# Optimization experiments

Hardware: AMD Instinct MI355X
Metric: run time of the kernel (lower is better)

## Reference

```python
import jax, jax.numpy as jnp
import numpy as np

EPS = 1e-5


def _bn(x, w, b, m, v):
    # eval-mode BatchNorm2d over channel axis (NCHW)
    inv = w / jnp.sqrt(v + EPS)
    return x * inv[None, :, None, None] + (b - m * inv)[None, :, None, None]


def _conv(x, w, pad):
    return jax.lax.conv_general_dilated(
        x, w, window_strides=(1, 1), padding=[(pad, pad), (pad, pad)],
        dimension_numbers=('NCHW', 'OIHW', 'NCHW'))


def setup_inputs() -> dict:
    key = jax.random.key(0)
    ks = jax.random.split(key, 40)
    B, Cin, Cm, Cout, H, W = 4, 64, 64, 64, 64, 64
    C8 = Cm // 8
    d = {}
    d['x'] = jax.random.normal(ks[0], (B, Cin, H, W), jnp.float32)
    d['conv1_w'] = jax.random.normal(ks[1], (Cm, Cin, 3, 3), jnp.float32) * 0.05
    d['conv2_w'] = jax.random.normal(ks[2], (Cout, Cm, 3, 3), jnp.float32) * 0.05

    def bn_params(i, c):
        return (jax.random.normal(ks[i], (c,), jnp.float32) * 0.1 + 1.0,
                jax.random.normal(ks[i + 1], (c,), jnp.float32) * 0.1,
                jax.random.normal(ks[i + 2], (c,), jnp.float32) * 0.1,
                jax.random.uniform(ks[i + 3], (c,), jnp.float32) + 0.5)

    d['f_w'] = jax.random.normal(ks[3], (C8, Cm, 1, 1), jnp.float32) * 0.1
    d['f_b'] = jax.random.normal(ks[4], (C8,), jnp.float32) * 0.05
    d['f_bn_w'], d['f_bn_b'], d['f_bn_m'], d['f_bn_v'] = bn_params(5, C8)
    d['g_w'] = jax.random.normal(ks[9], (C8, Cm, 1, 1), jnp.float32) * 0.1
    d['g_b'] = jax.random.normal(ks[10], (C8,), jnp.float32) * 0.05
    d['g_bn_w'], d['g_bn_b'], d['g_bn_m'], d['g_bn_v'] = bn_params(11, C8)
    d['gamma'] = jax.random.normal(ks[15], (1,), jnp.float32) * 0.5
    d['h_w'] = jax.random.normal(ks[16], (C8, Cm, 1, 1), jnp.float32) * 0.1
    d['h_b'] = jax.random.normal(ks[17], (C8,), jnp.float32) * 0.05
    d['h_bn_w'], d['h_bn_b'], d['h_bn_m'], d['h_bn_v'] = bn_params(18, C8)
    d['i_w'] = jax.random.normal(ks[22], (Cm, C8, 1, 1), jnp.float32) * 0.1
    d['i_b'] = jax.random.normal(ks[23], (Cm,), jnp.float32) * 0.05
    d['i_bn_w'], d['i_bn_b'], d['i_bn_m'], d['i_bn_v'] = bn_params(24, Cm)
    return d


def reference(x, conv1_w, conv2_w,
              f_w, f_b, f_bn_w, f_bn_b, f_bn_m, f_bn_v,
              g_w, g_b, g_bn_w, g_bn_b, g_bn_m, g_bn_v,
              gamma, h_w, h_b, h_bn_w, h_bn_b, h_bn_m, h_bn_v,
              i_w, i_b, i_bn_w, i_bn_b, i_bn_m, i_bn_v):
    out = _conv(x, conv1_w, 1)                      # [B, Cm, W, H]
    B, Cm, Wd, Hd = out.shape
    C8 = Cm // 8
    N = Wd * Hd

    # SelfAttention: f/g 1x1-conv + BN projections -> [B,N,N] map, softmax over dim=1
    f = _bn(_conv(out, f_w, 0) + f_b[None, :, None, None], f_bn_w, f_bn_b, f_bn_m, f_bn_v)
    g = _bn(_conv(out, g_w, 0) + g_b[None, :, None, None], g_bn_w, g_bn_b, g_bn_m, g_bn_v)
    f = f.reshape(B, C8, N).transpose(0, 2, 1)      # [B, N, C8]
    g = g.reshape(B, C8, N)                         # [B, C8, N]
    att = jnp.einsum('bnc,bcm->bnm', f, g)          # [B, N, N]
    att = jax.nn.softmax(att, axis=1)               # torch softmax(att, 1)

    # SelfAttentionPost: gamma-scaled value projection, bmm, expand, BN, residual
    h = gamma * _bn(_conv(out, h_w, 0) + h_b[None, :, None, None], h_bn_w, h_bn_b, h_bn_m, h_bn_v)
    h = h.reshape(B, C8, N).transpose(0, 2, 1)      # [B, N, C8]
    h = jnp.einsum('bnm,bmc->bnc', att, h)          # [B, N, C8]
    h = h.reshape(B, Wd, Hd, C8).transpose(0, 3, 1, 2)  # [B, C8, W, H]
    out = _bn(_conv(h, i_w, 0) + i_b[None, :, None, None], i_bn_w, i_bn_b, i_bn_m, i_bn_v) + out

    return _conv(out, conv2_w, 1)
```

## Files before the change

### kernel.cpp

```cpp
#include <hip/hip_runtime.h>

#define EPSBN 1e-5f
#define L2E 1.44269504088896340736f

typedef __attribute__((ext_vector_type(4)))  float f32x4;
typedef __attribute__((ext_vector_type(16))) float f32x16;
typedef __attribute__((ext_vector_type(8)))  short bf16x8;

__device__ __forceinline__ unsigned short f2bf(float f) {
    unsigned u = __float_as_uint(f);
    u = (u + 0x7FFFu + ((u >> 16) & 1u)) >> 16;
    return (unsigned short)u;
}
__device__ __forceinline__ float bf2f(unsigned short h) {
    return __uint_as_float((unsigned)h << 16);
}
__device__ __forceinline__ unsigned cvt_pk_bf16(float lo, float hi) {
    unsigned r;
    asm("v_cvt_pk_bf16_f32 %0, %1, %2" : "=v"(r) : "v"(lo), "v"(hi));
    return r;
}

__global__ __launch_bounds__(256) void prep_k(
    const float* __restrict__ x, const float* __restrict__ w1,
    const float* __restrict__ w2,
    unsigned short* __restrict__ xT, unsigned short* __restrict__ wt1,
    unsigned short* __restrict__ wt2)
{
    const int tid = threadIdx.x;
    if (blockIdx.x < 256) {
        __shared__ unsigned short tls[64][72];
        const int b = blockIdx.x >> 6, p0 = (blockIdx.x & 63) << 6;
        const int ci = tid >> 2, pq = tid & 3;
        const float* src = x + (((size_t)(b * 64 + ci)) << 12) + p0 + pq * 16;
#pragma unroll
        for (int j = 0; j < 4; ++j) {
            const float4 v = *(const float4*)(src + j * 4);
            const int pl = pq * 16 + j * 4;
            tls[pl][ci]     = f2bf(v.x);
            tls[pl + 1][ci] = f2bf(v.y);
            tls[pl + 2][ci] = f2bf(v.z);
            tls[pl + 3][ci] = f2bf(v.w);
        }
        __syncthreads();
        const int pix = tid >> 2, cg = tid & 3;
        const uint4 a  = *(const uint4*)&tls[pix][cg << 4];
        const uint4 b2 = *(const uint4*)&tls[pix][(cg << 4) + 8];
        unsigned short* dst = xT + (((size_t)((b << 12) + p0 + pix)) << 6) + (cg << 4);
        *(uint4*)dst       = a;
        *(uint4*)(dst + 8) = b2;
    } else {
        const int e0 = (blockIdx.x - 256) * 2048 + tid * 8;
#pragma unroll
        for (int j = 0; j < 8; ++j) {
            const int e = e0 + j;
            const int which = e >= 36864;
            const int je = which ? e - 36864 : e;
            const int t_ = je >> 12, co = (je >> 6) & 63, ci = je & 63;
            const float val = (which ? w2 : w1)[(co * 64 + ci) * 9 + t_];
            (which ? wt2 : wt1)[je] = f2bf(val);
        }
    }
}

__global__ __launch_bounds__(256) void conv3x3_k(
    const unsigned short* __restrict__ xT, const unsigned short* __restrict__ wt,
    float* __restrict__ y)
{
    __shared__ unsigned short xs[3][66][72];
    __shared__ unsigned short ws[9][32][72];
    __shared__ float          ls[32][68];

    const int b  = blockIdx.z;
    const int cg = blockIdx.y;
    const int r0 = blockIdx.x;
    const int tid = threadIdx.x;

    for (int u = tid; u < 1536; u += 256) {
        const int kh = u >> 9, rem = u & 511;
        const int p = 1 + (rem >> 3), cig = rem & 7;
        const int gr = r0 + kh - 1;
        uint4 v = make_uint4(0u, 0u, 0u, 0u);
        if ((unsigned)gr < 64u)
            v = *(const uint4*)(xT + (((size_t)((b << 12) + (gr << 6) + (p - 1))) << 6) + (cig << 3));
        const int s = (p >> 3) & 7;
        *(uint4*)&xs[kh][p][(cig ^ s) << 3] = v;
    }
    if (tid < 48) {
        const int kh = tid >> 4, pp = (tid & 8) ? 65 : 0, cig = tid & 7;
        *(uint4*)&xs[kh][pp][cig << 3] = make_uint4(0u, 0u, 0u, 0u);
    }
    for (int u = tid; u < 2304; u += 256) {
        const int t_ = u >> 8, rem = u & 255;
        const int co = rem >> 3, cig = rem & 7;
        const uint4 v = *(const uint4*)(wt + (((t_ * 64) + (cg << 5) + co) << 6) + (cig << 3));
        *(uint4*)&ws[t_][co][cig << 3] = v;
    }
    __syncthreads();

    const int lane = tid & 63, grp = tid >> 6;
    const int lr = lane & 15, lk = lane >> 4;
    const int pixbase = (grp << 4) + lr;

    f32x4 acc0 = {0.f, 0.f, 0.f, 0.f};
    f32x4 acc1 = {0.f, 0.f, 0.f, 0.f};

#pragma unroll
    for (int t = 0; t < 9; ++t) {
        const int kh = t / 3, kw = t % 3;
        const int p  = pixbase + kw;
        const int sw = ((p >> 3) & 7) << 3;
#pragma unroll
        for (int ch = 0; ch < 2; ++ch) {
            const int cio = (ch << 5) + (lk << 3);
            const bf16x8 a  = *(const bf16x8*)&xs[kh][p][cio ^ sw];
            const bf16x8 b0 = *(const bf16x8*)&ws[t][lr][cio];
            const bf16x8 b1 = *(const bf16x8*)&ws[t][16 + lr][cio];
            acc0 = __builtin_amdgcn_mfma_f32_16x16x32_bf16(a, b0, acc0, 0, 0, 0);
            acc1 = __builtin_amdgcn_mfma_f32_16x16x32_bf16(a, b1, acc1, 0, 0, 0);
        }
    }

#pragma unroll
    for (int j = 0; j < 4; ++j) {
        const int pix = (grp << 4) + (lk << 2) + j;
        ls[lr][pix]      = acc0[j];
        ls[lr + 16][pix] = acc1[j];
    }
    __syncthreads();

    const int co_l = tid >> 3, pq = (tid & 7) << 3;
    float* yp = y + (((size_t)((b << 6) + (cg << 5) + co_l)) << 12) + (r0 << 6) + pq;
    *(float4*)yp       = *(const float4*)&ls[co_l][pq];
    *(float4*)(yp + 4) = *(const float4*)&ls[co_l][pq + 4];
}

__global__ __launch_bounds__(256) void proj_k(
    const float* __restrict__ out1,
    const float* __restrict__ f_w, const float* __restrict__ f_b,
    const float* __restrict__ f_bw, const float* __restrict__ f_bb,
    const float* __restrict__ f_bm, const float* __restrict__ f_bv,
    const float* __restrict__ g_w, const float* __restrict__ g_b,
    const float* __restrict__ g_bw, const float* __restrict__ g_bb,
    const float* __restrict__ g_bm, const float* __restrict__ g_bv,
    const float* __restrict__ h_w, const float* __restrict__ h_b,
    const float* __restrict__ h_bw, const float* __restrict__ h_bb,
    const float* __restrict__ h_bm, const float* __restrict__ h_bv,
    const float* __restrict__ gamma,
    unsigned short* __restrict__ fb, unsigned short* __restrict__ gb,
    float* __restrict__ hb)
{
    __shared__ float comb[3][64][25];

    const int pl = threadIdx.x >> 2, q = threadIdx.x & 3;
    const int pix = blockIdx.x * 64 + pl;
    const int b = pix >> 12, p = pix & 4095;
    const int cibase = q << 4;

    const float* xp = out1 + ((size_t)b << 18) + ((size_t)cibase << 12) + p;

    float aF[8], aG[8], aH[8];
#pragma unroll
    for (int c = 0; c < 8; ++c) { aF[c] = 0.f; aG[c] = 0.f; aH[c] = 0.f; }

#pragma unroll
    for (int ci = 0; ci < 16; ++ci) {
        const float xv = xp[(size_t)ci << 12];
#pragma unroll
        for (int c = 0; c < 8; ++c) {
            aF[c] = fmaf(xv, f_w[c * 64 + cibase + ci], aF[c]);
            aG[c] = fmaf(xv, g_w[c * 64 + cibase + ci], aG[c]);
            aH[c] = fmaf(xv, h_w[c * 64 + cibase + ci], aH[c]);
        }
    }

    if (q) {
        float* cp = comb[q - 1][pl];
#pragma unroll
        for (int c = 0; c < 8; ++c) { cp[c] = aF[c]; cp[8 + c] = aG[c]; cp[16 + c] = aH[c]; }
    }
    __syncthreads();
    if (q == 0) {
#pragma unroll
        for (int k = 0; k < 3; ++k) {
            const float* cp = comb[k][pl];
#pragma unroll
            for (int c = 0; c < 8; ++c) { aF[c] += cp[c]; aG[c] += cp[8 + c]; aH[c] += cp[16 + c]; }
        }

        const float gm = gamma[0];
        float fo[8], go[8], ho[8];
#pragma unroll
        for (int c = 0; c < 8; ++c) {
            float invf = f_bw[c] * rsqrtf(f_bv[c] + EPSBN);
            fo[c] = ((aF[c] + f_b[c]) * invf + (f_bb[c] - f_bm[c] * invf)) * L2E;
            float invg = g_bw[c] * rsqrtf(g_bv[c] + EPSBN);
            go[c] = (aG[c] + g_b[c]) * invg + (g_bb[c] - g_bm[c] * invg);
            float invh = h_bw[c] * rsqrtf(h_bv[c] + EPSBN);
            ho[c] = gm * ((aH[c] + h_b[c]) * invh + (h_bb[c] - h_bm[c] * invh));
        }

        unsigned short fhi[8], flo[8], ghi[8], glo[8];
#pragma unroll
        for (int c = 0; c < 8; ++c) {
            fhi[c] = f2bf(fo[c]);
            flo[c] = f2bf(fo[c] - bf2f(fhi[c]));
            ghi[c] = f2bf(go[c]);
            glo[c] = f2bf(go[c] - bf2f(ghi[c]));
        }
        uint4 fA, fB, gA, gB;
        fA.x = (unsigned)fhi[0] | ((unsigned)fhi[1] << 16);
        fA.y = (unsigned)fhi[2] | ((unsigned)fhi[3] << 16);
        fA.z = (unsigned)fhi[4] | ((unsigned)fhi[5] << 16);
        fA.w = (unsigned)fhi[6] | ((unsigned)fhi[7] << 16);
        fB.x = (unsigned)flo[0] | ((unsigned)flo[1] << 16);
        fB.y = (unsigned)flo[2] | ((unsigned)flo[3] << 16);
        fB.z = (unsigned)flo[4] | ((unsigned)flo[5] << 16);
        fB.w = (unsigned)flo[6] | ((unsigned)flo[7] << 16);
        gA.x = (unsigned)ghi[0] | ((unsigned)ghi[1] << 16);
        gA.y = (unsigned)ghi[2] | ((unsigned)ghi[3] << 16);
        gA.z = (unsigned)ghi[4] | ((unsigned)ghi[5] << 16);
        gA.w = (unsigned)ghi[6] | ((unsigned)ghi[7] << 16);
        gB.x = (unsigned)glo[0] | ((unsigned)glo[1] << 16);
        gB.y = (unsigned)glo[2] | ((unsigned)glo[3] << 16);
        gB.z = (unsigned)glo[4] | ((unsigned)glo[5] << 16);
        gB.w = (unsigned)glo[6] | ((unsigned)glo[7] << 16);

        *(uint4*)(fb + ((size_t)pix << 4))     = fA;
        *(uint4*)(fb + ((size_t)pix << 4) + 8) = fB;
        *(uint4*)(gb + ((size_t)pix << 4))     = gA;
        *(uint4*)(gb + ((size_t)pix << 4) + 8) = gB;

        float4* hp = (float4*)(hb + ((size_t)pix << 3));
        hp[0] = make_float4(ho[0], ho[1], ho[2], ho[3]);
        hp[1] = make_float4(ho[4], ho[5], ho[6], ho[7]);
    }
}

__global__ __launch_bounds__(256) void pass1_k(
    const unsigned short* __restrict__ fb, const unsigned short* __restrict__ gb,
    const float* __restrict__ hb, unsigned short* __restrict__ hT)
{
    __shared__ float Dp[4][2][16];
    __shared__ float Dscale[32];

    const int b = blockIdx.y;
    const int mtile0 = blockIdx.x << 5;
    const int tid = threadIdx.x;
    const int wv = tid >> 6, l = tid & 63, col = l & 31, hl = l >> 5;

    const bf16x8 Gf = *(const bf16x8*)(gb + (((size_t)(b * 4096 + mtile0 + col)) << 4) + (hl << 3));

    const f32x16 Z = {0.f, 0.f, 0.f, 0.f, 0.f, 0.f, 0.f, 0.f,
                      0.f, 0.f, 0.f, 0.f, 0.f, 0.f, 0.f, 0.f};
    float Dacc[16];
#pragma unroll
    for (int r = 0; r < 16; ++r) Dacc[r] = 0.f;

    const unsigned short* fbase = fb + (((size_t)(b * 4096 + (wv << 10))) << 4);

    for (int nc = 0; nc < 32; ++nc) {
        const unsigned short* fr = fbase + ((size_t)((nc << 5) + col) << 4);
        const bf16x8 Fhi = *(const bf16x8*)fr;
        const bf16x8 Flo = *(const bf16x8*)(fr + 8);
        f32x16 T = __builtin_amdgcn_mfma_f32_32x32x16_bf16(Gf, Fhi, Z, 0, 0, 0);
        T = __builtin_amdgcn_mfma_f32_32x32x16_bf16(Gf, Flo, T, 0, 0, 0);
#pragma unroll
        for (int r = 0; r < 16; ++r)
            Dacc[r] += __builtin_amdgcn_exp2f(T[r]);
    }

#pragma unroll
    for (int s = 1; s < 32; s <<= 1) {
#pragma unroll
        for (int r = 0; r < 16; ++r)
            Dacc[r] += __shfl_xor(Dacc[r], s);
    }

    if (col == 0) {
#pragma unroll
        for (int r = 0; r < 16; ++r) Dp[wv][hl][r] = Dacc[r];
    }
    __syncthreads();
    if (tid < 32) {
        const int r = tid & 15, h = tid >> 4;
        const float D = Dp[0][h][r] + Dp[1][h][r] + Dp[2][h][r] + Dp[3][h][r];
        const int m = (r & 3) + ((r >> 2) << 3) + (h << 2);
        Dscale[m] = 1.f / D;
    }
    __syncthreads();
    if (tid < 64) {
        const int ml = tid & 31, c0 = (tid >> 5) << 2;
        const float sc = Dscale[ml];
        const float4 hv = *(const float4*)(hb + (((size_t)(b * 4096 + mtile0 + ml)) << 3) + c0);
        unsigned short* o = hT + ((size_t)b << 15) + mtile0 + ml;
        o[(size_t)(c0    ) << 12] = f2bf(hv.x * sc);
        o[(size_t)(c0 + 1) << 12] = f2bf(hv.y * sc);
        o[(size_t)(c0 + 2) << 12] = f2bf(hv.z * sc);
        o[(size_t)(c0 + 3) << 12] = f2bf(hv.w * sc);
    }
}

__global__ __launch_bounds__(256) void pass2_k(
    const unsigned short* __restrict__ fb, const unsigned short* __restrict__ gb,
    const unsigned short* __restrict__ hT, float* __restrict__ o)
{
    __shared__ float red[4][64][4];

    const int b = blockIdx.y, nt = blockIdx.x;
    const int tid = threadIdx.x, wv = tid >> 6, l = tid & 63;
    const int col = l & 31;
    const bool lo = l < 32;
    const int hl8 = lo ? 0 : 8;

    const unsigned short* frow = fb + (((size_t)(b * 4096 + (nt << 5) + col)) << 4);
    const bf16x8 Fhi = *(const bf16x8*)frow;
    const bf16x8 Flo = *(const bf16x8*)(frow + 8);

    const f32x16 Z = {0.f, 0.f, 0.f, 0.f, 0.f, 0.f, 0.f, 0.f,
                      0.f, 0.f, 0.f, 0.f, 0.f, 0.f, 0.f, 0.f};
    f32x16 Oacc = Z;

    const unsigned short* hbase = hT + ((size_t)b << 15) + ((size_t)col << 12) + hl8;
    const bool hvalid = col < 8;

    for (int mci = 0; mci < 32; ++mci) {
        const int mc = (wv << 5) + mci;
        const bf16x8 Gf = *(const bf16x8*)(gb + (((size_t)(b * 4096 + (mc << 5) + col)) << 4) + hl8);
        f32x16 T = __builtin_amdgcn_mfma_f32_32x32x16_bf16(Gf, Fhi, Z, 0, 0, 0);
        T = __builtin_amdgcn_mfma_f32_32x32x16_bf16(Gf, Flo, T, 0, 0, 0);

        unsigned w[8];
#pragma unroll
        for (int pp = 0; pp < 8; ++pp)
            w[pp] = cvt_pk_bf16(__builtin_amdgcn_exp2f(T[2 * pp]),
                                __builtin_amdgcn_exp2f(T[2 * pp + 1]));

        const unsigned ea = __shfl_xor(lo ? w[2] : w[0], 32);
        const unsigned eb = __shfl_xor(lo ? w[3] : w[1], 32);
        const unsigned ec = __shfl_xor(lo ? w[6] : w[4], 32);
        const unsigned ed = __shfl_xor(lo ? w[7] : w[5], 32);

        union { unsigned u[4]; bf16x8 v; } B1, B2;
        B1.u[0] = lo ? w[0] : ea;  B1.u[1] = lo ? w[1] : eb;
        B1.u[2] = lo ? ea   : w[2]; B1.u[3] = lo ? eb   : w[3];
        B2.u[0] = lo ? w[4] : ec;  B2.u[1] = lo ? w[5] : ed;
        B2.u[2] = lo ? ec   : w[6]; B2.u[3] = lo ? ed   : w[7];

        bf16x8 A1 = {0, 0, 0, 0, 0, 0, 0, 0};
        bf16x8 A2 = {0, 0, 0, 0, 0, 0, 0, 0};
        if (hvalid) {
            A1 = *(const bf16x8*)(hbase + (mc << 5));
            A2 = *(const bf16x8*)(hbase + (mc << 5) + 16);
        }
        Oacc = __builtin_amdgcn_mfma_f32_32x32x16_bf16(A1, B1.v, Oacc, 0, 0, 0);
        Oacc = __builtin_amdgcn_mfma_f32_32x32x16_bf16(A2, B2.v, Oacc, 0, 0, 0);
    }

    *(float4*)&red[wv][l][0] = make_float4(Oacc[0], Oacc[1], Oacc[2], Oacc[3]);
    __syncthreads();
    if (tid < 64) {
        const float4 s0 = *(const float4*)&red[0][tid][0];
        const float4 s1 = *(const float4*)&red[1][tid][0];
        const float4 s2 = *(const float4*)&red[2][tid][0];
        const float4 s3 = *(const float4*)&red[3][tid][0];
        const float4 s = make_float4(s0.x + s1.x + s2.x + s3.x,
                                     s0.y + s1.y + s2.y + s3.y,
                                     s0.z + s1.z + s2.z + s3.z,
                                     s0.w + s1.w + s2.w + s3.w);
        float* op = o + (((size_t)(b * 4096 + (nt << 5) + (tid & 31))) << 3) + ((tid >> 5) << 2);
        *(float4*)op = s;
    }
}

__global__ __launch_bounds__(256) void post_k(
    const float* __restrict__ o, const float* __restrict__ out1,
    const float* __restrict__ i_w, const float* __restrict__ i_b,
    const float* __restrict__ i_bw, const float* __restrict__ i_bb,
    const float* __restrict__ i_bm, const float* __restrict__ i_bv,
    unsigned short* __restrict__ out2T)
{
    __shared__ float          os[64][12];
    __shared__ unsigned short ls[64][72];

    const int b = blockIdx.y, p0 = blockIdx.x << 6;
    const int tid = threadIdx.x;

    if (tid < 128) {
        const int pix = tid >> 1, hf = tid & 1;
        *(float4*)&os[pix][hf * 4] =
            *(const float4*)(o + (((size_t)(b * 4096 + p0 + pix)) << 3) + hf * 4);
    }
    __syncthreads();

    const int co = tid >> 2, pq = tid & 3;
    const float inv = i_bw[co] * rsqrtf(i_bv[co] + EPSBN);
    const float bs  = i_b[co] * inv + i_bb[co] - i_bm[co] * inv;
    float iw[8];
#pragma unroll
    for (int c = 0; c < 8; ++c) iw[c] = i_w[co * 8 + c] * inv;

    const float* o1p = out1 + (((size_t)(b * 64 + co)) << 12) + p0 + pq * 16;
#pragma unroll
    for (int k = 0; k < 16; ++k) {
        const int pix = pq * 16 + k;
        const float4 oa = *(const float4*)&os[pix][0];
        const float4 ob = *(const float4*)&os[pix][4];
        const float v = oa.x * iw[0] + oa.y * iw[1] + oa.z * iw[2] + oa.w * iw[3]
                      + ob.x * iw[4] + ob.y * iw[5] + ob.z * iw[6] + ob.w * iw[7];
        ls[pix][co] = f2bf(v + bs + o1p[k]);
    }
    __syncthreads();

    const int pix = tid >> 2, cg = tid & 3;
    const uint4 a  = *(const uint4*)&ls[pix][cg << 4];
    const uint4 b2 = *(const uint4*)&ls[pix][(cg << 4) + 8];
    unsigned short* dst = out2T + (((size_t)(b * 4096 + p0 + pix)) << 6) + (cg << 4);
    *(uint4*)dst       = a;
    *(uint4*)(dst + 8) = b2;
}

extern "C" void kernel_launch(void* const* d_in, const int* in_sizes, int n_in,
                              void* d_out, int out_size, void* d_ws, size_t ws_size,
                              hipStream_t stream) {
    const float* x       = (const float*)d_in[0];
    const float* conv1_w = (const float*)d_in[1];
    const float* conv2_w = (const float*)d_in[2];
    const float* f_w  = (const float*)d_in[3];
    const float* f_b  = (const float*)d_in[4];
    const float* f_bw = (const float*)d_in[5];
    const float* f_bb = (const float*)d_in[6];
    const float* f_bm = (const float*)d_in[7];
    const float* f_bv = (const float*)d_in[8];
    const float* g_w  = (const float*)d_in[9];
    const float* g_b  = (const float*)d_in[10];
    const float* g_bw = (const float*)d_in[11];
    const float* g_bb = (const float*)d_in[12];
    const float* g_bm = (const float*)d_in[13];
    const float* g_bv = (const float*)d_in[14];
    const float* gamma = (const float*)d_in[15];
    const float* h_w  = (const float*)d_in[16];
    const float* h_b  = (const float*)d_in[17];
    const float* h_bw = (const float*)d_in[18];
    const float* h_bb = (const float*)d_in[19];
    const float* h_bm = (const float*)d_in[20];
    const float* h_bv = (const float*)d_in[21];
    const float* i_w  = (const float*)d_in[22];
    const float* i_b  = (const float*)d_in[23];
    const float* i_bw = (const float*)d_in[24];
    const float* i_bb = (const float*)d_in[25];
    const float* i_bm = (const float*)d_in[26];
    const float* i_bv = (const float*)d_in[27];

    float* ws = (float*)d_ws;
    float* out1 = ws;
    unsigned short* xT    = (unsigned short*)(ws + 1048576);
    unsigned short* fbuf  = (unsigned short*)(ws + 1572864);
    unsigned short* gbuf  = (unsigned short*)(ws + 1703936);
    float* hbuf = ws + 1835008;
    unsigned short* hT    = (unsigned short*)(ws + 1966080);
    unsigned short* wt1   = (unsigned short*)(ws + 2031616);
    unsigned short* wt2   = (unsigned short*)(ws + 2050048);
    unsigned short* out2T = (unsigned short*)(ws + 2068480);
    float* obuf = hbuf;

    prep_k<<<292, 256, 0, stream>>>(x, conv1_w, conv2_w, xT, wt1, wt2);

    conv3x3_k<<<dim3(64, 2, 4), 256, 0, stream>>>(xT, wt1, out1);

    proj_k<<<256, 256, 0, stream>>>(out1,
        f_w, f_b, f_bw, f_bb, f_bm, f_bv,
        g_w, g_b, g_bw, g_bb, g_bm, g_bv,
        h_w, h_b, h_bw, h_bb, h_bm, h_bv,
        gamma, fbuf, gbuf, hbuf);

    pass1_k<<<dim3(128, 4), 256, 0, stream>>>(fbuf, gbuf, hbuf, hT);

    pass2_k<<<dim3(128, 4), 256, 0, stream>>>(fbuf, gbuf, hT, obuf);

    post_k<<<dim3(64, 4), 256, 0, stream>>>(obuf, out1,
        i_w, i_b, i_bw, i_bb, i_bm, i_bv, out2T);

    conv3x3_k<<<dim3(64, 2, 4), 256, 0, stream>>>(out2T, wt2, (float*)d_out);
}
```

Baseline: 82.64 us.

## Fuse post-attention projection into pass2 and keep conv weights in registers

The post_k kernel (1x1 expansion conv, BN, residual add, bf16 transpose) is folded into the tail of pass2_k. This removes one kernel launch and the float round-trip of the attention output through global memory. Separately, conv3x3_k now loads its weight fragments straight from global memory into registers instead of staging them in shared memory. That frees LDS but adds 36 bf16x8 registers per thread, which may lower occupancy.

```diff
diff --git a/kernel.cpp b/kernel.cpp
--- a/kernel.cpp
+++ b/kernel.cpp
@@ -68,13 +68,24 @@
     float* __restrict__ y)
 {
     __shared__ unsigned short xs[3][66][72];
-    __shared__ unsigned short ws[9][32][72];
     __shared__ float          ls[32][68];
 
     const int b  = blockIdx.z;
     const int cg = blockIdx.y;
     const int r0 = blockIdx.x;
     const int tid = threadIdx.x;
+    const int lane = tid & 63, grp = tid >> 6;
+    const int lr = lane & 15, lk = lane >> 4;
+
+    bf16x8 w0[9][2], w1[9][2];
+#pragma unroll
+    for (int t = 0; t < 9; ++t)
+#pragma unroll
+        for (int ch = 0; ch < 2; ++ch) {
+            const int cio = (ch << 5) + (lk << 3);
+            w0[t][ch] = *(const bf16x8*)(wt + (((t * 64) + (cg << 5) + lr) << 6) + cio);
+            w1[t][ch] = *(const bf16x8*)(wt + (((t * 64) + (cg << 5) + 16 + lr) << 6) + cio);
+        }
 
     for (int u = tid; u < 1536; u += 256) {
         const int kh = u >> 9, rem = u & 511;
@@ -90,16 +101,8 @@
         const int kh = tid >> 4, pp = (tid & 8) ? 65 : 0, cig = tid & 7;
         *(uint4*)&xs[kh][pp][cig << 3] = make_uint4(0u, 0u, 0u, 0u);
     }
-    for (int u = tid; u < 2304; u += 256) {
-        const int t_ = u >> 8, rem = u & 255;
-        const int co = rem >> 3, cig = rem & 7;
-        const uint4 v = *(const uint4*)(wt + (((t_ * 64) + (cg << 5) + co) << 6) + (cig << 3));
-        *(uint4*)&ws[t_][co][cig << 3] = v;
-    }
-    __syncthreads();
-
-    const int lane = tid & 63, grp = tid >> 6;
-    const int lr = lane & 15, lk = lane >> 4;
+    __syncthreads();
+
     const int pixbase = (grp << 4) + lr;
 
     f32x4 acc0 = {0.f, 0.f, 0.f, 0.f};
@@ -113,11 +116,9 @@
 #pragma unroll
         for (int ch = 0; ch < 2; ++ch) {
             const int cio = (ch << 5) + (lk << 3);
-            const bf16x8 a  = *(const bf16x8*)&xs[kh][p][cio ^ sw];
-            const bf16x8 b0 = *(const bf16x8*)&ws[t][lr][cio];
-            const bf16x8 b1 = *(const bf16x8*)&ws[t][16 + lr][cio];
-            acc0 = __builtin_amdgcn_mfma_f32_16x16x32_bf16(a, b0, acc0, 0, 0, 0);
-            acc1 = __builtin_amdgcn_mfma_f32_16x16x32_bf16(a, b1, acc1, 0, 0, 0);
+            const bf16x8 a = *(const bf16x8*)&xs[kh][p][cio ^ sw];
+            acc0 = __builtin_amdgcn_mfma_f32_16x16x32_bf16(a, w0[t][ch], acc0, 0, 0, 0);
+            acc1 = __builtin_amdgcn_mfma_f32_16x16x32_bf16(a, w1[t][ch], acc1, 0, 0, 0);
         }
     }
 
@@ -303,9 +304,16 @@
 
 __global__ __launch_bounds__(256) void pass2_k(
     const unsigned short* __restrict__ fb, const unsigned short* __restrict__ gb,
-    const unsigned short* __restrict__ hT, float* __restrict__ o)
+    const unsigned short* __restrict__ hT,
+    const float* __restrict__ out1,
+    const float* __restrict__ i_w, const float* __restrict__ i_b,
+    const float* __restrict__ i_bw, const float* __restrict__ i_bb,
+    const float* __restrict__ i_bm, const float* __restrict__ i_bv,
+    unsigned short* __restrict__ out2T)
 {
     __shared__ float red[4][64][4];
+    __shared__ float os[32][8];
+    __shared__ unsigned short ls[32][72];
 
     const int b = blockIdx.y, nt = blockIdx.x;
     const int tid = threadIdx.x, wv = tid >> 6, l = tid & 63;
@@ -364,60 +372,45 @@
         const float4 s1 = *(const float4*)&red[1][tid][0];
         const float4 s2 = *(const float4*)&red[2][tid][0];
         const float4 s3 = *(const float4*)&red[3][tid][0];
-        const float4 s = make_float4(s0.x + s1.x + s2.x + s3.x,
-                                     s0.y + s1.y + s2.y + s3.y,
-                                     s0.z + s1.z + s2.z + s3.z,
-                                     s0.w + s1.w + s2.w + s3.w);
-        float* op = o + (((size_t)(b * 4096 + (nt << 5) + (tid & 31))) << 3) + ((tid >> 5) << 2);
-        *(float4*)op = s;
-    }
-}
-
-__global__ __launch_bounds__(256) void post_k(
-    const float* __restrict__ o, const float* __restrict__ out1,
-    const float* __restrict__ i_w, const float* __restrict__ i_b,
-    const float* __restrict__ i_bw, const float* __restrict__ i_bb,
-    const float* __restrict__ i_bm, const float* __restrict__ i_bv,
-    unsigned short* __restrict__ out2T)
-{
-    __shared__ float          os[64][12];
-    __shared__ unsigned short ls[64][72];
-
-    const int b = blockIdx.y, p0 = blockIdx.x << 6;
-    const int tid = threadIdx.x;
-
+        *(float4*)&os[tid & 31][(tid >> 5) << 2] =
+            make_float4(s0.x + s1.x + s2.x + s3.x,
+                        s0.y + s1.y + s2.y + s3.y,
+                        s0.z + s1.z + s2.z + s3.z,
+                        s0.w + s1.w + s2.w + s3.w);
+    }
+    __syncthreads();
+
+    {
+        const int co = tid & 63, pg = tid >> 6;
+        const int p0 = nt << 5;
+        const float inv = i_bw[co] * rsqrtf(i_bv[co] + EPSBN);
+        const float bs  = i_b[co] * inv + i_bb[co] - i_bm[co] * inv;
+        float iw[8];
+#pragma unroll
+        for (int c = 0; c < 8; ++c) iw[c] = i_w[co * 8 + c] * inv;
+
+        const float* o1p = out1 + (((size_t)(b * 64 + co)) << 12) + p0 + pg * 8;
+        const float4 r1 = *(const float4*)o1p;
+        const float4 r2 = *(const float4*)(o1p + 4);
+        const float rv[8] = {r1.x, r1.y, r1.z, r1.w, r2.x, r2.y, r2.z, r2.w};
+
+#pragma unroll
+        for (int k = 0; k < 8; ++k) {
+            const int pix = pg * 8 + k;
+            const float4 oa = *(const float4*)&os[pix][0];
+            const float4 ob = *(const float4*)&os[pix][4];
+            const float v = oa.x * iw[0] + oa.y * iw[1] + oa.z * iw[2] + oa.w * iw[3]
+                          + ob.x * iw[4] + ob.y * iw[5] + ob.z * iw[6] + ob.w * iw[7];
+            ls[pix][co] = f2bf(v + bs + rv[k]);
+        }
+    }
+    __syncthreads();
     if (tid < 128) {
-        const int pix = tid >> 1, hf = tid & 1;
-        *(float4*)&os[pix][hf * 4] =
-            *(const float4*)(o + (((size_t)(b * 4096 + p0 + pix)) << 3) + hf * 4);
-    }
-    __syncthreads();
-
-    const int co = tid >> 2, pq = tid & 3;
-    const float inv = i_bw[co] * rsqrtf(i_bv[co] + EPSBN);
-    const float bs  = i_b[co] * inv + i_bb[co] - i_bm[co] * inv;
-    float iw[8];
-#pragma unroll
-    for (int c = 0; c < 8; ++c) iw[c] = i_w[co * 8 + c] * inv;
-
-    const float* o1p = out1 + (((size_t)(b * 64 + co)) << 12) + p0 + pq * 16;
-#pragma unroll
-    for (int k = 0; k < 16; ++k) {
-        const int pix = pq * 16 + k;
-        const float4 oa = *(const float4*)&os[pix][0];
-        const float4 ob = *(const float4*)&os[pix][4];
-        const float v = oa.x * iw[0] + oa.y * iw[1] + oa.z * iw[2] + oa.w * iw[3]
-                      + ob.x * iw[4] + ob.y * iw[5] + ob.z * iw[6] + ob.w * iw[7];
-        ls[pix][co] = f2bf(v + bs + o1p[k]);
-    }
-    __syncthreads();
-
-    const int pix = tid >> 2, cg = tid & 3;
-    const uint4 a  = *(const uint4*)&ls[pix][cg << 4];
-    const uint4 b2 = *(const uint4*)&ls[pix][(cg << 4) + 8];
-    unsigned short* dst = out2T + (((size_t)(b * 4096 + p0 + pix)) << 6) + (cg << 4);
-    *(uint4*)dst       = a;
-    *(uint4*)(dst + 8) = b2;
+        const int pix = tid >> 2, cgi = tid & 3;
+        unsigned short* dst = out2T + (((size_t)(b * 4096 + (nt << 5) + pix)) << 6) + (cgi << 4);
+        *(uint4*)dst       = *(const uint4*)&ls[pix][cgi << 4];
+        *(uint4*)(dst + 8) = *(const uint4*)&ls[pix][(cgi << 4) + 8];
+    }
 }
 
 extern "C" void kernel_launch(void* const* d_in, const int* in_sizes, int n_in,
@@ -462,7 +455,6 @@
     unsigned short* wt1   = (unsigned short*)(ws + 2031616);
     unsigned short* wt2   = (unsigned short*)(ws + 2050048);
     unsigned short* out2T = (unsigned short*)(ws + 2068480);
-    float* obuf = hbuf;
 
     prep_k<<<292, 256, 0, stream>>>(x, conv1_w, conv2_w, xT, wt1, wt2);
 
@@ -476,9 +468,7 @@
 
     pass1_k<<<dim3(128, 4), 256, 0, stream>>>(fbuf, gbuf, hbuf, hT);
 
-    pass2_k<<<dim3(128, 4), 256, 0, stream>>>(fbuf, gbuf, hT, obuf);
-
-    post_k<<<dim3(64, 4), 256, 0, stream>>>(obuf, out1,
+    pass2_k<<<dim3(128, 4), 256, 0, stream>>>(fbuf, gbuf, hT, out1,
         i_w, i_b, i_bw, i_bb, i_bm, i_bv, out2T);
 
     conv3x3_k<<<dim3(64, 2, 4), 256, 0, stream>>>(out2T, wt2, (float*)d_out);
```

Result: slower. 90.94 us (+10.0%).
